# Kernel tuning notes

Hardware: AMD Instinct MI355X
Metric: run time of the kernel (lower is better)

## Reference

```python
import jax, jax.numpy as jnp
import numpy as np

NH, DK, DV = 8, 10, 10  # num_heads, per-head key dim, per-head value dim (dim_k=dim_v=80)


def setup_inputs() -> dict:
    key = jax.random.key(0)
    k1, k2, k3, k4, k5 = jax.random.split(key, 5)
    B, NX, NY = 64, 512, 512
    x = jax.random.normal(k1, (B, NX, 768), dtype=jnp.float32)
    y = jax.random.normal(k2, (B, NY, 283), dtype=jnp.float32)
    # nn.Linear(bias=False) weights, stored transposed as (in, out); scaled init
    Wq = jax.random.normal(k3, (768, 80), dtype=jnp.float32) * 0.02
    Wk = jax.random.normal(k4, (283, 80), dtype=jnp.float32) * 0.02
    Wv = jax.random.normal(k5, (283, 80), dtype=jnp.float32) * 0.02
    return {"x": x, "y": y, "Wq": Wq, "Wk": Wk, "Wv": Wv}


def reference(x, y, Wq, Wk, Wv):
    B, nx, _ = x.shape
    ny = y.shape[1]
    # projections -> split heads: (B, nh, seq, dhead)
    q = (x @ Wq).reshape(B, nx, NH, DK).transpose(0, 2, 1, 3)
    k = (y @ Wk).reshape(B, ny, NH, DK).transpose(0, 2, 1, 3)
    v = (y @ Wv).reshape(B, ny, NH, DV).transpose(0, 2, 1, 3)
    scale = 1.0 / np.sqrt(DK).astype(np.float32)
    dist = jax.nn.softmax(jnp.einsum("bhqd,bhkd->bhqk", q, k) * scale, axis=-1)
    att = q + jnp.einsum("bhqk,bhkd->bhqd", dist, v)  # residual add of q
    att = att.transpose(0, 2, 1, 3).reshape(B, nx, NH * DV)
    # module returns `result` = flattened attention (fc/BN stack is dead code)
    return att.reshape(B, -1)
```

## Files before the change

kernel.cpp:

```cpp
#include <hip/hip_runtime.h>
#include <stdint.h>

typedef unsigned short u16;
typedef unsigned int   u32;
typedef _Float16       f16;

typedef __attribute__((ext_vector_type(2))) _Float16 half2v;
typedef __attribute__((ext_vector_type(4))) _Float16 half4v;
typedef __attribute__((ext_vector_type(8))) _Float16 half8v;
typedef __attribute__((ext_vector_type(4))) float    floatx4;

#define NXS    512
#define NYS    512
#define NHEAD  8
#define DHEAD  10
#define DMODEL 80
#define DXK    768
#define DYK    283
#define DYKP   288

__device__ inline half2v pk2(float x, float y) {
  return __builtin_bit_cast(half2v, __builtin_amdgcn_cvt_pkrtz(x, y));
}
__device__ inline half4v cvt4(float4 v) {
  return __builtin_shufflevector(pk2(v.x, v.y), pk2(v.z, v.w), 0, 1, 2, 3);
}
__device__ inline half4v h4u32(u32 a, u32 b) {
  return __builtin_shufflevector(__builtin_bit_cast(half2v, a),
                                 __builtin_bit_cast(half2v, b), 0, 1, 2, 3);
}

__global__ __launch_bounds__(256) void w_prep(const float* __restrict__ Wq,
                                              const float* __restrict__ Wk,
                                              const float* __restrict__ Wv,
                                              f16* __restrict__ Tq,
                                              f16* __restrict__ Tk,
                                              f16* __restrict__ Tv) {
  const int idx = blockIdx.x * 256 + threadIdx.x;
  if (idx < 80 * 768) {
    const int c = idx / 768, k = idx - c * 768;
    Tq[idx] = (f16)Wq[k * 80 + c];
  }
  if (idx < 80 * 288) {
    const int c = idx / 288, k = idx - c * 288;
    float a = 0.f, b = 0.f;
    if (k < DYK) { a = Wk[k * 80 + c]; b = Wv[k * 80 + c]; }
    Tk[idx] = (f16)a;
    Tv[idx] = (f16)b;
  }
}

__global__ __launch_bounds__(256) void proj(const float* __restrict__ X,
                                            const float* __restrict__ Y,
                                            const f16* __restrict__ Wtq,
                                            const f16* __restrict__ Wtk,
                                            const f16* __restrict__ Wtv,
                                            f16* __restrict__ Qw,
                                            f16* __restrict__ Kw,
                                            f16* __restrict__ Vw) {
  const int t = threadIdx.x;
  const int wv = t >> 6, lane = t & 63, m16 = lane & 15, quad = lane >> 4;
  const int blk = blockIdx.x;

  if (blk < 512) {
    const int rowb = blk * 64 + wv * 16;
    const float* xr = X + (size_t)(rowb + m16) * DXK + quad * 8;
    const f16* wb = Wtq + (size_t)m16 * DXK + quad * 8;

    floatx4 acc[5];
#pragma unroll
    for (int i = 0; i < 5; ++i) acc[i] = (floatx4){0.f, 0.f, 0.f, 0.f};

#pragma unroll 4
    for (int s = 0; s < 24; ++s) {
      const int k0 = s * 32;
      const float4 x0 = *(const float4*)(xr + k0);
      const float4 x1 = *(const float4*)(xr + k0 + 4);
      const half8v a = __builtin_shufflevector(cvt4(x0), cvt4(x1),
                                               0, 1, 2, 3, 4, 5, 6, 7);
#pragma unroll
      for (int nt = 0; nt < 5; ++nt) {
        const half8v b = *(const half8v*)(wb + (size_t)nt * 16 * DXK + k0);
        acc[nt] = __builtin_amdgcn_mfma_f32_16x16x32_f16(a, b, acc[nt], 0, 0, 0);
      }
    }
#pragma unroll
    for (int nt = 0; nt < 5; ++nt) {
      const int col = nt * 16 + m16;
#pragma unroll
      for (int p = 0; p < 4; ++p)
        Qw[(size_t)(rowb + quad * 4 + p) * DMODEL + col] = (f16)acc[nt][p];
    }
  } else {
    const int rowb = (blk - 512) * 64 + wv * 16;
    const float* yr = Y + (size_t)(rowb + m16) * DYK + quad * 8;
    const f16* wbk = Wtk + (size_t)m16 * DYKP + quad * 8;
    const f16* wbv = Wtv + (size_t)m16 * DYKP + quad * 8;

    floatx4 ak[5], av[5];
#pragma unroll
    for (int i = 0; i < 5; ++i) {
      ak[i] = (floatx4){0.f, 0.f, 0.f, 0.f};
      av[i] = (floatx4){0.f, 0.f, 0.f, 0.f};
    }

#pragma unroll 2
    for (int s = 0; s < 9; ++s) {
      const int k0 = s * 32;
      float y8[8];
      if (s < 8) {
#pragma unroll
        for (int j = 0; j < 8; ++j) y8[j] = yr[k0 + j];
      } else {
#pragma unroll
        for (int j = 0; j < 8; ++j) {
          const int k = k0 + quad * 8 + j;
          y8[j] = (k < DYK) ? yr[k0 + j] : 0.f;
        }
      }
      const half8v a = __builtin_shufflevector(
          cvt4((float4){y8[0], y8[1], y8[2], y8[3]}),
          cvt4((float4){y8[4], y8[5], y8[6], y8[7]}), 0, 1, 2, 3, 4, 5, 6, 7);
#pragma unroll
      for (int nt = 0; nt < 5; ++nt) {
        const half8v bk = *(const half8v*)(wbk + (size_t)nt * 16 * DYKP + k0);
        ak[nt] = __builtin_amdgcn_mfma_f32_16x16x32_f16(a, bk, ak[nt], 0, 0, 0);
        const half8v bv = *(const half8v*)(wbv + (size_t)nt * 16 * DYKP + k0);
        av[nt] = __builtin_amdgcn_mfma_f32_16x16x32_f16(a, bv, av[nt], 0, 0, 0);
      }
    }
#pragma unroll
    for (int nt = 0; nt < 5; ++nt) {
      const int col = nt * 16 + m16;
      const int h = col / 10, d = col - h * 10;
#pragma unroll
      for (int p = 0; p < 4; ++p) {
        const int grow = rowb + quad * 4 + p;
        const int bb = grow >> 9, ny = grow & 511;
        const size_t o = (((size_t)bb * NHEAD + h) * NYS + ny) * DHEAD + d;
        Kw[o] = (f16)ak[nt][p];
        Vw[o] = (f16)av[nt][p];
      }
    }
  }
}

__global__ __launch_bounds__(256) void attn(const f16* __restrict__ Q,
                                            const f16* __restrict__ K,
                                            const f16* __restrict__ V,
                                            float* __restrict__ O) {
  __shared__ f16 Ks[512 * 22];
  __shared__ f16 Vt[16 * 522];
  const int t = threadIdx.x;
  const int wv = t >> 6, lane = t & 63, m16 = lane & 15, quad = lane >> 4;
  const int bh = blockIdx.x >> 1, half = blockIdx.x & 1;
  const int b = bh >> 3, h = bh & 7;

  const u32* Kg = (const u32*)K + (size_t)bh * NYS * 5;
  const u32* Vg = (const u32*)V + (size_t)bh * NYS * 5;
  for (int idx = t; idx < 2560; idx += 256) {
    const u32 row = (u32)idx / 5u, c = (u32)idx - row * 5u;
    const half2v kv = __builtin_bit_cast(half2v, Kg[idx]);
    Ks[row * 22 + 2 * c]     = kv[0];
    Ks[row * 22 + 2 * c + 1] = kv[1];
    const half2v vv = __builtin_bit_cast(half2v, Vg[idx]);
    Vt[(2 * c) * 522 + row]     = vv[0];
    Vt[(2 * c + 1) * 522 + row] = vv[1];
  }
  for (int idx = t; idx < 3072; idx += 256) {
    const u32 row = (u32)idx / 6u, d = 10u + ((u32)idx - row * 6u);
    Ks[row * 22 + d] = (f16)0.f;
  }
  for (int idx = t; idx < 6 * 522; idx += 256)
    Vt[10 * 522 + idx] = (f16)0.f;
  __syncthreads();

  const float scale = 0.31622776601683794f;
#pragma unroll 1
  for (int i = 0; i < 4; ++i) {
    const int qt = half * 16 + wv * 4 + i;
    const int qrow = qt * 16 + m16;
    const u32* Qg32 = (const u32*)(Q + ((size_t)b * NXS + qrow) * DMODEL + h * DHEAD);
    float s0 = 0.f, s1 = 0.f, s2 = 0.f, s3 = 0.f;
    if (quad < 2) {
      const u32 ua = Qg32[quad * 2], ub = Qg32[quad * 2 + 1];
      const half2v ha = __builtin_bit_cast(half2v, ua);
      const half2v hb = __builtin_bit_cast(half2v, ub);
      s0 = (float)ha[0]; s1 = (float)ha[1]; s2 = (float)hb[0]; s3 = (float)hb[1];
    } else if (quad == 2) {
      const u32 ua = Qg32[4];
      const half2v ha = __builtin_bit_cast(half2v, ua);
      s0 = (float)ha[0]; s1 = (float)ha[1];
    }
    const half4v qf = __builtin_shufflevector(pk2(s0 * scale, s1 * scale),
                                              pk2(s2 * scale, s3 * scale),
                                              0, 1, 2, 3);
    floatx4 o0 = (floatx4){0.f, 0.f, 0.f, 0.f};
    floatx4 o1 = (floatx4){0.f, 0.f, 0.f, 0.f};
    float l0 = 0.f, l1 = 0.f;
    for (int kt = 0; kt < 32; kt += 2) {
#pragma unroll
      for (int u = 0; u < 2; ++u) {
        const int ktu = kt + u;
        const int kb = (ktu * 16 + m16) * 22 + quad * 4;
        const half4v kf = h4u32(*(const u32*)&Ks[kb], *(const u32*)&Ks[kb + 2]);
        const floatx4 s = __builtin_amdgcn_mfma_f32_16x16x16f16(
            kf, qf, (floatx4){0.f, 0.f, 0.f, 0.f}, 0, 0, 0);
        const float p0 = __expf(s[0]);
        const float p1 = __expf(s[1]);
        const float p2 = __expf(s[2]);
        const float p3 = __expf(s[3]);
        const half4v pf = __builtin_shufflevector(pk2(p0, p1), pk2(p2, p3),
                                                  0, 1, 2, 3);
        const int vb = m16 * 522 + ktu * 16 + quad * 4;
        const half4v vf = h4u32(*(const u32*)&Vt[vb], *(const u32*)&Vt[vb + 2]);
        if (u == 0) {
          l0 += (p0 + p1) + (p2 + p3);
          o0 = __builtin_amdgcn_mfma_f32_16x16x16f16(pf, vf, o0, 0, 0, 0);
        } else {
          l1 += (p0 + p1) + (p2 + p3);
          o1 = __builtin_amdgcn_mfma_f32_16x16x16f16(pf, vf, o1, 0, 0, 0);
        }
      }
    }
    float lp = l0 + l1;
    lp += __shfl_xor(lp, 16);
    lp += __shfl_xor(lp, 32);
#pragma unroll
    for (int p = 0; p < 4; ++p) {
      const int rq = qt * 16 + quad * 4 + p;
      const float lr = __shfl(lp, quad * 4 + p);
      if (m16 < DHEAD) {
        const float qres = (float)Q[((size_t)b * NXS + rq) * DMODEL + h * DHEAD + m16];
        O[((size_t)b * NXS + rq) * DMODEL + h * DHEAD + m16] =
            qres + (o0[p] + o1[p]) / lr;
      }
    }
  }
}

extern "C" void kernel_launch(void* const* d_in, const int* in_sizes, int n_in,
                              void* d_out, int out_size, void* d_ws, size_t ws_size,
                              hipStream_t stream) {
  const float* x  = (const float*)d_in[0];
  const float* y  = (const float*)d_in[1];
  const float* Wq = (const float*)d_in[2];
  const float* Wk = (const float*)d_in[3];
  const float* Wv = (const float*)d_in[4];
  float* out = (float*)d_out;

  char* ws = (char*)d_ws;
  f16* Wtq = (f16*)(ws);
  f16* Wtk = (f16*)(ws + 122880);
  f16* Wtv = (f16*)(ws + 168960);
  f16* Qw  = (f16*)(ws + 262144);
  f16* Kw  = (f16*)(ws + 5505024);
  f16* Vw  = (f16*)(ws + 10747904);

  w_prep<<<240, 256, 0, stream>>>(Wq, Wk, Wv, Wtq, Wtk, Wtv);
  proj  <<<1024, 256, 0, stream>>>(x, y, Wtq, Wtk, Wtv, Qw, Kw, Vw);
  attn  <<<1024, 256, 0, stream>>>(Qw, Kw, Vw, out);
}
```

Baseline: 265.0 us.

## Stage projection X/Y and weight tiles through LDS with register prefetch

The projection kernel now loads each 32-wide K slice of the input rows and the weight matrices cooperatively, with coalesced loads, into padded shared-memory tiles. The next slice is prefetched into registers while the MFMAs run on the current one. Before this, each lane read strided rows straight from global memory and every wave re-read the weights. The cost is two barriers per K step and extra LDS traffic, and the Y path now uses scalar per-element loads.

```diff
diff --git a/kernel.cpp b/kernel.cpp
--- a/kernel.cpp
+++ b/kernel.cpp
@@ -63,24 +63,47 @@
   const int blk = blockIdx.x;
 
   if (blk < 512) {
-    const int rowb = blk * 64 + wv * 16;
-    const float* xr = X + (size_t)(rowb + m16) * DXK + quad * 8;
-    const f16* wb = Wtq + (size_t)m16 * DXK + quad * 8;
+    __shared__ f16 Xs[64 * 40];
+    __shared__ f16 Ws[80 * 40];
+    const int row0 = blk * 64;
+    const int xr_r = t >> 3, xr_k = (t & 7) << 2;
+    const int wi0 = t, wi1 = t + 160;
+
+    float4 xr0, xr1;
+    uint4 wr0, wr1;
+    xr0 = *(const float4*)&X[(size_t)(row0 + xr_r) * DXK + xr_k];
+    xr1 = *(const float4*)&X[(size_t)(row0 + xr_r + 32) * DXK + xr_k];
+    if (t < 160) {
+      wr0 = *(const uint4*)&Wtq[(wi0 >> 2) * DXK + (wi0 & 3) * 8];
+      wr1 = *(const uint4*)&Wtq[(wi1 >> 2) * DXK + (wi1 & 3) * 8];
+    }
 
     floatx4 acc[5];
 #pragma unroll
     for (int i = 0; i < 5; ++i) acc[i] = (floatx4){0.f, 0.f, 0.f, 0.f};
 
-#pragma unroll 4
     for (int s = 0; s < 24; ++s) {
-      const int k0 = s * 32;
-      const float4 x0 = *(const float4*)(xr + k0);
-      const float4 x1 = *(const float4*)(xr + k0 + 4);
-      const half8v a = __builtin_shufflevector(cvt4(x0), cvt4(x1),
-                                               0, 1, 2, 3, 4, 5, 6, 7);
+      if (s) __syncthreads();
+      *(half4v*)&Xs[xr_r * 40 + xr_k] = cvt4(xr0);
+      *(half4v*)&Xs[(xr_r + 32) * 40 + xr_k] = cvt4(xr1);
+      if (t < 160) {
+        *(uint4*)&Ws[(wi0 >> 2) * 40 + (wi0 & 3) * 8] = wr0;
+        *(uint4*)&Ws[(wi1 >> 2) * 40 + (wi1 & 3) * 8] = wr1;
+      }
+      __syncthreads();
+      if (s < 23) {
+        const int k0 = (s + 1) * 32;
+        xr0 = *(const float4*)&X[(size_t)(row0 + xr_r) * DXK + k0 + xr_k];
+        xr1 = *(const float4*)&X[(size_t)(row0 + xr_r + 32) * DXK + k0 + xr_k];
+        if (t < 160) {
+          wr0 = *(const uint4*)&Wtq[(wi0 >> 2) * DXK + k0 + (wi0 & 3) * 8];
+          wr1 = *(const uint4*)&Wtq[(wi1 >> 2) * DXK + k0 + (wi1 & 3) * 8];
+        }
+      }
+      const half8v a = *(const half8v*)&Xs[(wv * 16 + m16) * 40 + quad * 8];
 #pragma unroll
       for (int nt = 0; nt < 5; ++nt) {
-        const half8v b = *(const half8v*)(wb + (size_t)nt * 16 * DXK + k0);
+        const half8v b = *(const half8v*)&Ws[(nt * 16 + m16) * 40 + quad * 8];
         acc[nt] = __builtin_amdgcn_mfma_f32_16x16x32_f16(a, b, acc[nt], 0, 0, 0);
       }
     }
@@ -88,14 +111,32 @@
     for (int nt = 0; nt < 5; ++nt) {
       const int col = nt * 16 + m16;
 #pragma unroll
-      for (int p = 0; p < 4; ++p)
-        Qw[(size_t)(rowb + quad * 4 + p) * DMODEL + col] = (f16)acc[nt][p];
+      for (int p = 0; p < 4; ++p) {
+        const int grow = row0 + wv * 16 + quad * 4 + p;
+        Qw[(size_t)grow * DMODEL + col] = (f16)acc[nt][p];
+      }
     }
   } else {
-    const int rowb = (blk - 512) * 64 + wv * 16;
-    const float* yr = Y + (size_t)(rowb + m16) * DYK + quad * 8;
-    const f16* wbk = Wtk + (size_t)m16 * DYKP + quad * 8;
-    const f16* wbv = Wtv + (size_t)m16 * DYKP + quad * 8;
+    __shared__ f16 Ys[64 * 40];
+    __shared__ f16 Wks[80 * 40];
+    __shared__ f16 Wvs[80 * 40];
+    const int row0 = (blk - 512) * 64;
+    const int wi0 = t, wi1 = t + 160;
+
+    float yr[8];
+    uint4 wk0, wk1, wv0, wv1;
+#pragma unroll
+    for (int i = 0; i < 8; ++i) {
+      const int idx = t + 256 * i;
+      const int r = idx >> 5, kk = idx & 31;
+      yr[i] = Y[(size_t)(row0 + r) * DYK + kk];
+    }
+    if (t < 160) {
+      wk0 = *(const uint4*)&Wtk[(wi0 >> 2) * DYKP + (wi0 & 3) * 8];
+      wk1 = *(const uint4*)&Wtk[(wi1 >> 2) * DYKP + (wi1 & 3) * 8];
+      wv0 = *(const uint4*)&Wtv[(wi0 >> 2) * DYKP + (wi0 & 3) * 8];
+      wv1 = *(const uint4*)&Wtv[(wi1 >> 2) * DYKP + (wi1 & 3) * 8];
+    }
 
     floatx4 ak[5], av[5];
 #pragma unroll
@@ -104,28 +145,41 @@
       av[i] = (floatx4){0.f, 0.f, 0.f, 0.f};
     }
 
-#pragma unroll 2
     for (int s = 0; s < 9; ++s) {
-      const int k0 = s * 32;
-      float y8[8];
+      if (s) __syncthreads();
+#pragma unroll
+      for (int i = 0; i < 8; ++i) {
+        const int idx = t + 256 * i;
+        Ys[(idx >> 5) * 40 + (idx & 31)] = (f16)yr[i];
+      }
+      if (t < 160) {
+        *(uint4*)&Wks[(wi0 >> 2) * 40 + (wi0 & 3) * 8] = wk0;
+        *(uint4*)&Wks[(wi1 >> 2) * 40 + (wi1 & 3) * 8] = wk1;
+        *(uint4*)&Wvs[(wi0 >> 2) * 40 + (wi0 & 3) * 8] = wv0;
+        *(uint4*)&Wvs[(wi1 >> 2) * 40 + (wi1 & 3) * 8] = wv1;
+      }
+      __syncthreads();
       if (s < 8) {
-#pragma unroll
-        for (int j = 0; j < 8; ++j) y8[j] = yr[k0 + j];
-      } else {
-#pragma unroll
-        for (int j = 0; j < 8; ++j) {
-          const int k = k0 + quad * 8 + j;
-          y8[j] = (k < DYK) ? yr[k0 + j] : 0.f;
+        const int k0 = (s + 1) * 32;
+#pragma unroll
+        for (int i = 0; i < 8; ++i) {
+          const int idx = t + 256 * i;
+          const int r = idx >> 5, k = k0 + (idx & 31);
+          yr[i] = (k < DYK) ? Y[(size_t)(row0 + r) * DYK + k] : 0.f;
         }
-      }
-      const half8v a = __builtin_shufflevector(
-          cvt4((float4){y8[0], y8[1], y8[2], y8[3]}),
-          cvt4((float4){y8[4], y8[5], y8[6], y8[7]}), 0, 1, 2, 3, 4, 5, 6, 7);
+        if (t < 160) {
+          wk0 = *(const uint4*)&Wtk[(wi0 >> 2) * DYKP + k0 + (wi0 & 3) * 8];
+          wk1 = *(const uint4*)&Wtk[(wi1 >> 2) * DYKP + k0 + (wi1 & 3) * 8];
+          wv0 = *(const uint4*)&Wtv[(wi0 >> 2) * DYKP + k0 + (wi0 & 3) * 8];
+          wv1 = *(const uint4*)&Wtv[(wi1 >> 2) * DYKP + k0 + (wi1 & 3) * 8];
+        }
+      }
+      const half8v a = *(const half8v*)&Ys[(wv * 16 + m16) * 40 + quad * 8];
 #pragma unroll
       for (int nt = 0; nt < 5; ++nt) {
-        const half8v bk = *(const half8v*)(wbk + (size_t)nt * 16 * DYKP + k0);
+        const half8v bk = *(const half8v*)&Wks[(nt * 16 + m16) * 40 + quad * 8];
         ak[nt] = __builtin_amdgcn_mfma_f32_16x16x32_f16(a, bk, ak[nt], 0, 0, 0);
-        const half8v bv = *(const half8v*)(wbv + (size_t)nt * 16 * DYKP + k0);
+        const half8v bv = *(const half8v*)&Wvs[(nt * 16 + m16) * 40 + quad * 8];
         av[nt] = __builtin_amdgcn_mfma_f32_16x16x32_f16(a, bv, av[nt], 0, 0, 0);
       }
     }
@@ -135,7 +189,7 @@
       const int h = col / 10, d = col - h * 10;
 #pragma unroll
       for (int p = 0; p < 4; ++p) {
-        const int grow = rowb + quad * 4 + p;
+        const int grow = row0 + wv * 16 + quad * 4 + p;
         const int bb = grow >> 9, ny = grow & 511;
         const size_t o = (((size_t)bb * NHEAD + h) * NYS + ny) * DHEAD + d;
         Kw[o] = (f16)ak[nt][p];
@@ -163,9 +217,9 @@
     const half2v kv = __builtin_bit_cast(half2v, Kg[idx]);
     Ks[row * 22 + 2 * c]     = kv[0];
     Ks[row * 22 + 2 * c + 1] = kv[1];
-    const half2v vv = __builtin_bit_cast(half2v, Vg[idx]);
-    Vt[(2 * c) * 522 + row]     = vv[0];
-    Vt[(2 * c + 1) * 522 + row] = vv[1];
+    const half2v vvv = __builtin_bit_cast(half2v, Vg[idx]);
+    Vt[(2 * c) * 522 + row]     = vvv[0];
+    Vt[(2 * c + 1) * 522 + row] = vvv[1];
   }
   for (int idx = t; idx < 3072; idx += 256) {
     const u32 row = (u32)idx / 6u, d = 10u + ((u32)idx - row * 6u);
```

After: 237.0 us. -10.6%, faster.
